# Kernel optimization log

Measured on AMD Instinct MI355X. Metric: run time of the kernel, lower is better.

Reference implementation:

```python
import jax, jax.numpy as jnp
import numpy as np

B, L, D_EMB, D_K, D_V, N_HEAD = 32, 512, 768, 512, 1024, 8
LN_EPS = 1e-6
MASK_FILL = 1e-9  # non-standard fill value from the original module


def setup_inputs() -> dict:
    key = jax.random.key(0)
    ks = jax.random.split(key, 13)
    s = 0.02
    return {
        "q": jax.random.normal(ks[0], (B, L, D_EMB), jnp.float32),
        "k": jax.random.normal(ks[1], (B, L, D_EMB), jnp.float32),
        "v": jax.random.normal(ks[2], (B, L, D_EMB), jnp.float32),
        "Wq": jax.random.normal(ks[3], (D_EMB, D_K), jnp.float32) * s,
        "Wk": jax.random.normal(ks[4], (D_EMB, D_K), jnp.float32) * s,
        "Wv": jax.random.normal(ks[5], (D_EMB, D_V), jnp.float32) * s,
        "Wconv": jax.random.normal(ks[6], (D_K, D_K), jnp.float32) * s,  # Conv1d k=1 (out_ch, in_ch)
        "bconv": jax.random.normal(ks[7], (D_K,), jnp.float32) * s,
        "Wfc": jax.random.normal(ks[8], (D_V, D_EMB), jnp.float32) * s,
        "gamma": jnp.ones((D_EMB,), jnp.float32),
        "beta": jnp.zeros((D_EMB,), jnp.float32),
        "mask1": jax.random.randint(ks[9], (B, L), 0, 2).astype(jnp.bool_),
        "mask2": jax.random.randint(ks[10], (B, L), 0, 2).astype(jnp.bool_),
    }


def reference(q, k, v, Wq, Wk, Wv, Wconv, bconv, Wfc, gamma, beta, mask1, mask2):
    Bq, Lq, _ = q.shape
    Lk = k.shape[1]
    dh_k = D_K // N_HEAD
    dh_v = D_V // N_HEAD
    residual = q

    # Q/K projections followed by the (buggy-but-faithful) Conv1d(k=1) that
    # treats the sequence axis as channels: out[b,o,l] = sum_c W[o,c]*x[b,c,l] + bias[o]
    q1 = q @ Wq                                   # (B, Lq, D_K)
    k1 = k @ Wk                                   # (B, Lk, D_K)
    q1 = jnp.einsum('oc,bcl->bol', Wconv, q1) + bconv[None, :, None]
    k1 = jnp.einsum('oc,bcl->bol', Wconv, k1) + bconv[None, :, None]
    v1 = v @ Wv                                   # (B, Lk, D_V)

    qh = q1.reshape(Bq, Lq, N_HEAD, dh_k).transpose(0, 2, 1, 3)  # (B,H,Lq,dk/H)
    kh = k1.reshape(Bq, Lk, N_HEAD, dh_k).transpose(0, 2, 1, 3)
    vh = v1.reshape(Bq, Lk, N_HEAD, dh_v).transpose(0, 2, 1, 3)

    temp = jnp.sqrt(jnp.asarray(D_K, qh.dtype))
    attn = jnp.einsum('bhqd,bhkd->bhqk', qh / temp, kh)          # (B,H,Lq,Lk)
    attn = jnp.where(mask1[:, None, :, None], MASK_FILL, attn)
    attn = jnp.where(mask2[:, None, None, :], MASK_FILL, attn)
    attn = jax.nn.softmax(attn, axis=-1)
    # dropout is identity in eval / deterministic reference

    out = jnp.einsum('bhqk,bhkd->bhqd', attn, vh)                # (B,H,Lq,dv/H)
    out = out.transpose(0, 2, 1, 3).reshape(Bq, Lq, D_V)
    out = out @ Wfc + residual                                   # (B,Lq,D_EMB)

    mu = out.mean(-1, keepdims=True)
    var = out.var(-1, keepdims=True)
    out = (out - mu) / jnp.sqrt(var + LN_EPS) * gamma + beta
    out = jnp.where(jnp.isnan(out), jnp.zeros((), out.dtype), out)
    return out, attn
```

## Files before the change

kernel.cpp:

```cpp
#include <hip/hip_runtime.h>
#include <hip/hip_fp16.h>

typedef short v8s __attribute__((ext_vector_type(8)));
typedef short v4s __attribute__((ext_vector_type(4)));
typedef float v4f __attribute__((ext_vector_type(4)));

#define BM 128
#define BN 128
#define BK 64

__device__ __forceinline__ float b2f(unsigned short u) {
    union { unsigned int i; float f; } x; x.i = ((unsigned int)u) << 16; return x.f;
}
__device__ __forceinline__ unsigned short f2b(float f) {
    union { float f; unsigned int i; } x; x.f = f;
    unsigned int r = x.i + 0x7fffu + ((x.i >> 16) & 1u);
    return (unsigned short)(r >> 16);
}

__device__ __forceinline__ void gload16(const void* g, void* l) {
    __builtin_amdgcn_global_load_lds(
        (const __attribute__((address_space(1))) void*)g,
        (__attribute__((address_space(3))) void*)l, 16, 0, 0);
}

template<int EPI>
__global__ __launch_bounds__(256)
void gemm_bt(const unsigned short* __restrict__ A, int lda, long aSB,
             const unsigned short* __restrict__ BT, int ldb, long bSB,
             void* __restrict__ C, int ldc, long cSB,
             int K,
             const float* __restrict__ bias,
             const float* __restrict__ resid, int ldr)
{
    const int z = blockIdx.z;

    __shared__ unsigned short As[BM * BK];
    __shared__ unsigned short Bs[BN * BK];

    const int tid = threadIdx.x;
    const int wave = tid >> 6, lane = tid & 63;
    const int wm = (wave >> 1) * 64, wn = (wave & 1) * 64;
    const int quad = lane >> 4, l16 = lane & 15;
    const int sx = l16 & 7;
    const int bm = blockIdx.y * BM, bn = blockIdx.x * BN;

    const unsigned short* aP[4]; const unsigned short* bP[4];
    unsigned short* lA[4]; unsigned short* lB[4];
#pragma unroll
    for (int p = 0; p < 4; p++) {
        int idx = p * 256 + tid;
        int row = idx >> 3, c = idx & 7, cc = c ^ (row & 7);
        aP[p] = A + (long)z * aSB + (long)(bm + row) * lda + cc * 8;
        bP[p] = BT + (long)z * bSB + (long)(bn + row) * ldb + cc * 8;
        lA[p] = &As[idx * 8];
        lB[p] = &Bs[idx * 8];
    }

    v4f acc[4][4] = {};

    for (int k0 = 0; k0 < K; k0 += BK) {
#pragma unroll
        for (int p = 0; p < 4; p++) {
            gload16(aP[p] + k0, lA[p]);
            gload16(bP[p] + k0, lB[p]);
        }
        __syncthreads();
#pragma unroll
        for (int ks = 0; ks < 2; ks++) {
            v8s af[4], bf[4];
#pragma unroll
            for (int i = 0; i < 4; i++) {
                const int co = ((ks * 4 + quad) ^ sx) * 8;
                af[i] = *(const v8s*)&As[(wm + i * 16 + l16) * 64 + co];
                bf[i] = *(const v8s*)&Bs[(wn + i * 16 + l16) * 64 + co];
            }
#pragma unroll
            for (int i = 0; i < 4; i++)
#pragma unroll
                for (int j = 0; j < 4; j++)
                    acc[i][j] = __builtin_amdgcn_mfma_f32_16x16x32_bf16(af[i], bf[j], acc[i][j], 0, 0, 0);
        }
        __syncthreads();
    }

    unsigned short* Cu = (unsigned short*)C + (long)z * cSB;

#pragma unroll
    for (int i = 0; i < 4; i++) {
        int rowbase = wm + i * 16 + quad * 4;
#pragma unroll
        for (int j = 0; j < 4; j++) {
            int gn = bn + wn + j * 16 + l16;
#pragma unroll
            for (int r = 0; r < 4; r++) {
                int gm = bm + rowbase + r;
                float v = acc[i][j][r];
                if (EPI == 1) {
                    int bb = gm >> 9, mm = gm & 511;
                    ((unsigned short*)C)[(long)bb * cSB + (long)gn * ldc + mm] = f2b(v);
                } else if (EPI == 2) {
                    Cu[(long)gm * ldc + gn] = f2b(v + bias[gm]);
                } else if (EPI == 4) {
                    Cu[(long)gm * ldc + gn] = f2b(v + resid[(long)gm * ldr + gn]);
                }
            }
        }
    }
}

__global__ __launch_bounds__(512, 4)
void scores_pv_k(const unsigned short* __restrict__ q1c,
                 const unsigned short* __restrict__ k1c,
                 const unsigned short* __restrict__ v1t,
                 float* __restrict__ attn,
                 unsigned short* __restrict__ out1,
                 const int* __restrict__ mask1,
                 const int* __restrict__ mask2,
                 float scale)
{
    const int id = blockIdx.x;
    const int logical = (id & 7) * 128 + (id >> 3);
    const int z = logical >> 2;
    const int bx = logical & 3;
    const int b = z >> 3, h = z & 7;

    const unsigned short* Qb = q1c + (long)b * 262144 + h * 64;
    const unsigned short* Kb = k1c + (long)b * 262144 + h * 64;
    const unsigned short* Vb = v1t + (long)b * 524288 + (long)h * 65536;

    __shared__ unsigned short KA[128 * 64];
    __shared__ unsigned short VB[128 * 128];
    __shared__ unsigned short Pl[8][640];
    __shared__ int m2s[512];

    const int tid = threadIdx.x;
    const int wave = tid >> 6, lane = tid & 63;
    const int quad = lane >> 4, l16 = lane & 15;
    const int sx = l16 & 7;
    const int bm = bx * 128;
    const int row_l = wave * 16 + l16;
    const int qrow = bm + row_l;

    m2s[tid] = mask2[b * 512 + tid];

    v8s qf0 = *(const v8s*)&Qb[(long)qrow * 512 + quad * 8];
    v8s qf1 = *(const v8s*)&Qb[(long)qrow * 512 + 32 + quad * 8];
    const int m1 = mask1[b * 512 + qrow];

    float m_l = -1e30f, sum = 0.f;

    for (int kt = 0; kt < 4; kt++) {
#pragma unroll
        for (int p = 0; p < 2; p++) {
            int idx = p * 512 + tid;
            int row = idx >> 3, c = idx & 7, cc = c ^ (row & 7);
            gload16(Kb + (long)(kt * 128 + row) * 512 + cc * 8, &KA[idx * 8]);
        }
        __syncthreads();
#pragma unroll
        for (int jl = 0; jl < 8; jl++) {
            const unsigned short* kr = &KA[(jl * 16 + l16) * 64];
            v8s kf0 = *(const v8s*)&kr[(quad ^ sx) << 3];
            v8s kf1 = *(const v8s*)&kr[((4 + quad) ^ sx) << 3];
            v4f a = (v4f){0.f, 0.f, 0.f, 0.f};
            a = __builtin_amdgcn_mfma_f32_16x16x32_bf16(kf0, qf0, a, 0, 0, 0);
            a = __builtin_amdgcn_mfma_f32_16x16x32_bf16(kf1, qf1, a, 0, 0, 0);
            int j = kt * 8 + jl;
            int4 m2v = *(const int4*)&m2s[j * 16 + quad * 4];
            float s0 = (m1 != 0 || m2v.x != 0) ? 1e-9f : a[0] * scale;
            float s1 = (m1 != 0 || m2v.y != 0) ? 1e-9f : a[1] * scale;
            float s2 = (m1 != 0 || m2v.z != 0) ? 1e-9f : a[2] * scale;
            float s3 = (m1 != 0 || m2v.w != 0) ? 1e-9f : a[3] * scale;
            float m4 = fmaxf(fmaxf(s0, s1), fmaxf(s2, s3));
            float mn = fmaxf(m_l, m4);
            sum = sum * __expf(m_l - mn)
                + (__expf(s0 - mn) + __expf(s1 - mn))
                + (__expf(s2 - mn) + __expf(s3 - mn));
            m_l = mn;
        }
        __syncthreads();
    }
    float mx = fmaxf(m_l, __shfl_xor(m_l, 16, 64));
    mx = fmaxf(mx, __shfl_xor(mx, 32, 64));
    sum *= __expf(m_l - mx);
    sum += __shfl_xor(sum, 16, 64);
    sum += __shfl_xor(sum, 32, 64);
    const float inv = 1.0f / sum;

    float* Arow = attn + (long)z * 262144 + (long)qrow * 512;
    unsigned short* Pw = &Pl[wave][l16 * 40];
    v4f acc2[8];
#pragma unroll
    for (int t = 0; t < 8; t++) acc2[t] = (v4f){0.f, 0.f, 0.f, 0.f};

    for (int kt = 0; kt < 4; kt++) {
#pragma unroll
        for (int p = 0; p < 2; p++) {
            int idx = p * 512 + tid;
            int row = idx >> 3, c = idx & 7, cc = c ^ (row & 7);
            gload16(Kb + (long)(kt * 128 + row) * 512 + cc * 8, &KA[idx * 8]);
        }
#pragma unroll
        for (int p = 0; p < 4; p++) {
            int idx = p * 512 + tid;
            int dv = idx >> 4, c = idx & 15, cc = c ^ (dv & 7);
            gload16(Vb + (long)dv * 512 + kt * 128 + cc * 8, &VB[idx * 8]);
        }
        __syncthreads();

#pragma unroll
        for (int g = 0; g < 4; g++) {
            float p8[8];
#pragma unroll
            for (int t2 = 0; t2 < 2; t2++) {
                int jl = g * 2 + t2;
                const unsigned short* kr = &KA[(jl * 16 + l16) * 64];
                v8s kf0 = *(const v8s*)&kr[(quad ^ sx) << 3];
                v8s kf1 = *(const v8s*)&kr[((4 + quad) ^ sx) << 3];
                v4f a = (v4f){0.f, 0.f, 0.f, 0.f};
                a = __builtin_amdgcn_mfma_f32_16x16x32_bf16(kf0, qf0, a, 0, 0, 0);
                a = __builtin_amdgcn_mfma_f32_16x16x32_bf16(kf1, qf1, a, 0, 0, 0);
                int j = kt * 8 + jl;
                int4 m2v = *(const int4*)&m2s[j * 16 + quad * 4];
                float s0 = (m1 != 0 || m2v.x != 0) ? 1e-9f : a[0] * scale;
                float s1 = (m1 != 0 || m2v.y != 0) ? 1e-9f : a[1] * scale;
                float s2 = (m1 != 0 || m2v.z != 0) ? 1e-9f : a[2] * scale;
                float s3 = (m1 != 0 || m2v.w != 0) ? 1e-9f : a[3] * scale;
                p8[t2 * 4 + 0] = __expf(s0 - mx) * inv;
                p8[t2 * 4 + 1] = __expf(s1 - mx) * inv;
                p8[t2 * 4 + 2] = __expf(s2 - mx) * inv;
                p8[t2 * 4 + 3] = __expf(s3 - mx) * inv;
            }
            int j0 = kt * 8 + g * 2;
            float4 w0; w0.x = p8[0]; w0.y = p8[1]; w0.z = p8[2]; w0.w = p8[3];
            float4 w1; w1.x = p8[4]; w1.y = p8[5]; w1.z = p8[6]; w1.w = p8[7];
            *(float4*)&Arow[j0 * 16 + quad * 4] = w0;
            *(float4*)&Arow[(j0 + 1) * 16 + quad * 4] = w1;
            uint2 pr0, pr1;
            pr0.x = (unsigned int)f2b(p8[0]) | ((unsigned int)f2b(p8[1]) << 16);
            pr0.y = (unsigned int)f2b(p8[2]) | ((unsigned int)f2b(p8[3]) << 16);
            pr1.x = (unsigned int)f2b(p8[4]) | ((unsigned int)f2b(p8[5]) << 16);
            pr1.y = (unsigned int)f2b(p8[6]) | ((unsigned int)f2b(p8[7]) << 16);
            *(uint2*)&Pw[quad * 4] = pr0;
            *(uint2*)&Pw[16 + quad * 4] = pr1;
            v8s pf = *(const v8s*)&Pw[quad * 8];
#pragma unroll
            for (int t = 0; t < 8; t++) {
                v8s vf = *(const v8s*)&VB[(t * 16 + l16) * 128 + (((g * 4 + quad) ^ sx) << 3)];
                acc2[t] = __builtin_amdgcn_mfma_f32_16x16x32_bf16(vf, pf, acc2[t], 0, 0, 0);
            }
        }
        __syncthreads();
    }

    unsigned short* Orow = out1 + (long)b * 524288 + (long)qrow * 1024 + h * 128;
#pragma unroll
    for (int t = 0; t < 8; t++) {
        v4s o;
        o[0] = (short)f2b(acc2[t][0]); o[1] = (short)f2b(acc2[t][1]);
        o[2] = (short)f2b(acc2[t][2]); o[3] = (short)f2b(acc2[t][3]);
        *(v4s*)&Orow[t * 16 + quad * 4] = o;
    }
}

__global__ __launch_bounds__(256)
void prep_k(const float* __restrict__ Wq, const float* __restrict__ Wk,
            const float* __restrict__ Wv, const float* __restrict__ Wfc,
            const float* __restrict__ Wconv,
            const float* __restrict__ qf, const float* __restrict__ kf,
            const float* __restrict__ vf,
            unsigned short* __restrict__ WqT, unsigned short* __restrict__ WkT,
            unsigned short* __restrict__ WvT, unsigned short* __restrict__ WfcT,
            unsigned short* __restrict__ Wconv_b,
            unsigned short* __restrict__ qb, unsigned short* __restrict__ kb,
            unsigned short* __restrict__ vb)
{
    __shared__ float t[32][33];
    int blk = blockIdx.x, tid = threadIdx.x;
    if (blk < 2304) {
        const float* src; unsigned short* dst; int K, N, local;
        if (blk < 384)       { src = Wq;  dst = WqT;  K = 768;  N = 512;  local = blk; }
        else if (blk < 768)  { src = Wk;  dst = WkT;  K = 768;  N = 512;  local = blk - 384; }
        else if (blk < 1536) { src = Wv;  dst = WvT;  K = 768;  N = 1024; local = blk - 768; }
        else                 { src = Wfc; dst = WfcT; K = 1024; N = 768;  local = blk - 1536; }
        int nb32 = N >> 5;
        int kb32 = (local / nb32) * 32, nb = (local % nb32) * 32;
        int tx = tid & 31, ty = tid >> 5;
#pragma unroll
        for (int i = 0; i < 32; i += 8)
            t[ty + i][tx] = src[(long)(kb32 + ty + i) * N + nb + tx];
        __syncthreads();
#pragma unroll
        for (int i = 0; i < 32; i += 8)
            dst[(long)(nb + ty + i) * K + kb32 + tx] = f2b(t[tx][ty + i]);
    } else if (blk < 3328) {
        int i = (blk - 2304) * 256 + tid;
        Wconv_b[i] = f2b(Wconv[i]);
    } else {
        long t0 = (long)(blk - 3328) * 4096 + (long)tid * 16;
        const float* src; unsigned short* dst; long i = t0;
        if (t0 < 12582912L)       { src = qf; dst = qb; }
        else if (t0 < 25165824L)  { src = kf; dst = kb; i = t0 - 12582912L; }
        else                      { src = vf; dst = vb; i = t0 - 25165824L; }
        float4 a = *(const float4*)&src[i];
        float4 b4 = *(const float4*)&src[i + 4];
        float4 c4 = *(const float4*)&src[i + 8];
        float4 d4 = *(const float4*)&src[i + 12];
        v8s r0, r1;
        r0[0] = (short)f2b(a.x);  r0[1] = (short)f2b(a.y);
        r0[2] = (short)f2b(a.z);  r0[3] = (short)f2b(a.w);
        r0[4] = (short)f2b(b4.x); r0[5] = (short)f2b(b4.y);
        r0[6] = (short)f2b(b4.z); r0[7] = (short)f2b(b4.w);
        r1[0] = (short)f2b(c4.x); r1[1] = (short)f2b(c4.y);
        r1[2] = (short)f2b(c4.z); r1[3] = (short)f2b(c4.w);
        r1[4] = (short)f2b(d4.x); r1[5] = (short)f2b(d4.y);
        r1[6] = (short)f2b(d4.z); r1[7] = (short)f2b(d4.w);
        *(v8s*)&dst[i] = r0;
        *(v8s*)&dst[i + 8] = r1;
    }
}

__global__ __launch_bounds__(256)
void ln_k(const unsigned short* __restrict__ x,
          const float* __restrict__ gamma,
          const float* __restrict__ beta,
          float* __restrict__ out)
{
    long row = (long)blockIdx.x * 4 + (threadIdx.x >> 6);
    int lane = threadIdx.x & 63;
    const unsigned short* p = x + row * 768;
    v8s a = *(const v8s*)&p[lane * 8];
    v4s b4 = *(const v4s*)&p[512 + lane * 4];
    float v[12];
    float s = 0.f, s2 = 0.f;
#pragma unroll
    for (int j = 0; j < 8; j++) { v[j] = b2f((unsigned short)a[j]); s += v[j]; s2 += v[j] * v[j]; }
#pragma unroll
    for (int j = 0; j < 4; j++) { v[8 + j] = b2f((unsigned short)b4[j]); s += v[8 + j]; s2 += v[8 + j] * v[8 + j]; }
#pragma unroll
    for (int o = 32; o > 0; o >>= 1) { s += __shfl_xor(s, o, 64); s2 += __shfl_xor(s2, o, 64); }
    float mean = s * (1.0f / 768.0f);
    float var = s2 * (1.0f / 768.0f) - mean * mean;
    if (!(var >= 0.f)) var = 0.f;
    float rstd = rsqrtf(var + 1e-6f);
    float o12[12];
#pragma unroll
    for (int j = 0; j < 8; j++) {
        int c = lane * 8 + j;
        float o = (v[j] - mean) * rstd * gamma[c] + beta[c];
        union { float f; unsigned int i; } uu; uu.f = o;
        if ((uu.i & 0x7FFFFFFFu) > 0x7F800000u) uu.f = 0.f;
        o12[j] = uu.f;
    }
#pragma unroll
    for (int j = 0; j < 4; j++) {
        int c = 512 + lane * 4 + j;
        float o = (v[8 + j] - mean) * rstd * gamma[c] + beta[c];
        union { float f; unsigned int i; } uu; uu.f = o;
        if ((uu.i & 0x7FFFFFFFu) > 0x7F800000u) uu.f = 0.f;
        o12[8 + j] = uu.f;
    }
    float4 f0; f0.x = o12[0]; f0.y = o12[1]; f0.z = o12[2]; f0.w = o12[3];
    float4 f1; f1.x = o12[4]; f1.y = o12[5]; f1.z = o12[6]; f1.w = o12[7];
    float4 f2; f2.x = o12[8]; f2.y = o12[9]; f2.z = o12[10]; f2.w = o12[11];
    *(float4*)&out[row * 768 + lane * 8] = f0;
    *(float4*)&out[row * 768 + lane * 8 + 4] = f1;
    *(float4*)&out[row * 768 + 512 + lane * 4] = f2;
}

extern "C" void kernel_launch(void* const* d_in, const int* in_sizes, int n_in,
                              void* d_out, int out_size, void* d_ws, size_t ws_size,
                              hipStream_t stream)
{
    const float* q     = (const float*)d_in[0];
    const float* k     = (const float*)d_in[1];
    const float* v     = (const float*)d_in[2];
    const float* Wq    = (const float*)d_in[3];
    const float* Wk    = (const float*)d_in[4];
    const float* Wv    = (const float*)d_in[5];
    const float* Wconv = (const float*)d_in[6];
    const float* bconv = (const float*)d_in[7];
    const float* Wfc   = (const float*)d_in[8];
    const float* gamma = (const float*)d_in[9];
    const float* beta  = (const float*)d_in[10];
    const int* mask1   = (const int*)d_in[11];
    const int* mask2   = (const int*)d_in[12];

    float* out  = (float*)d_out;
    float* attn = out + 12582912;

    unsigned short* ws = (unsigned short*)d_ws;
    unsigned short* WqT     = ws;
    unsigned short* WkT     = ws + 393216;
    unsigned short* WvT     = ws + 786432;
    unsigned short* WfcT    = ws + 1572864;
    unsigned short* Wconv_b = ws + 2359296;
    unsigned short* q1c     = ws + 2621440;
    unsigned short* k1c     = ws + 11010048;
    unsigned short* v1t     = ws + 19398656;
    unsigned short* out2    = ws + 19398656;

    unsigned short* aScr = (unsigned short*)attn;
    unsigned short* q1t = aScr;
    unsigned short* k1t = aScr + 8388608;
    unsigned short* qb  = aScr + 16777216;
    unsigned short* kb  = aScr + 29360128;
    unsigned short* vb  = aScr + 41943040;
    unsigned short* out1 = (unsigned short*)out;

    prep_k<<<12544, 256, 0, stream>>>(Wq, Wk, Wv, Wfc, Wconv, q, k, v,
                                      WqT, WkT, WvT, WfcT, Wconv_b, qb, kb, vb);

    const float scale = 0.04419417382415922f;

    gemm_bt<1><<<dim3(4, 128, 1), 256, 0, stream>>>(
        qb, 768, 0, WqT, 768, 0, q1t, 512, 262144, 768, nullptr, nullptr, 0);
    gemm_bt<1><<<dim3(4, 128, 1), 256, 0, stream>>>(
        kb, 768, 0, WkT, 768, 0, k1t, 512, 262144, 768, nullptr, nullptr, 0);
    gemm_bt<1><<<dim3(8, 128, 1), 256, 0, stream>>>(
        vb, 768, 0, WvT, 768, 0, v1t, 512, 524288, 768, nullptr, nullptr, 0);

    gemm_bt<2><<<dim3(4, 4, 32), 256, 0, stream>>>(
        Wconv_b, 512, 0, q1t, 512, 262144, q1c, 512, 262144, 512, bconv, nullptr, 0);
    gemm_bt<2><<<dim3(4, 4, 32), 256, 0, stream>>>(
        Wconv_b, 512, 0, k1t, 512, 262144, k1c, 512, 262144, 512, bconv, nullptr, 0);

    scores_pv_k<<<1024, 512, 0, stream>>>(
        q1c, k1c, v1t, attn, out1, mask1, mask2, scale);

    gemm_bt<4><<<dim3(6, 128, 1), 256, 0, stream>>>(
        out1, 1024, 0, WfcT, 1024, 0, out2, 768, 0, 1024, nullptr, q, 768);

    ln_k<<<4096, 256, 0, stream>>>(out2, gamma, beta, out);
}
```

Before: 708.8 us.

## Double-buffer GEMM LDS, stage transposed epilogue through LDS, merge projection launches

Refactors the bf16 MFMA GEMM into a device body that double-buffers the A/B tiles in LDS, so the next K-tile's global loads overlap the current tile's MFMAs and one barrier per iteration is removed. The transposed-output epilogue (EPI 1) now stages results in padded shared memory and writes coalesced 16-byte rows instead of scattered 2-byte stores. The three Q/K/V projections are merged into one launch, with idle blocks returning early for the narrower Q/K outputs, and the two conv GEMMs are merged into one launch. This cuts launch count and improves memory efficiency, at the cost of doubling LDS to 64KB per block, which may lower occupancy.

New measurement: 721.3 us. Within noise of the previous version (+1.8%).

```diff
diff --git a/kernel.cpp b/kernel.cpp
--- a/kernel.cpp
+++ b/kernel.cpp
@@ -1,5 +1,4 @@
 #include <hip/hip_runtime.h>
-#include <hip/hip_fp16.h>
 
 typedef short v8s __attribute__((ext_vector_type(8)));
 typedef short v4s __attribute__((ext_vector_type(4)));
@@ -22,6 +21,123 @@
     __builtin_amdgcn_global_load_lds(
         (const __attribute__((address_space(1))) void*)g,
         (__attribute__((address_space(3))) void*)l, 16, 0, 0);
+}
+
+template<int EPI>
+__device__ __forceinline__ void gemm_body(
+    const unsigned short* __restrict__ A, int lda, long aOff,
+    const unsigned short* __restrict__ BT, int ldb, long bOff,
+    void* __restrict__ C, int ldc, long cOff, long cSBt,
+    int K, const float* __restrict__ bias,
+    const float* __restrict__ resid, int ldr,
+    int bm, int bn)
+{
+    __shared__ unsigned short SM[32768];
+
+    const int tid = threadIdx.x;
+    const int wave = tid >> 6, lane = tid & 63;
+    const int wm = (wave >> 1) * 64, wn = (wave & 1) * 64;
+    const int quad = lane >> 4, l16 = lane & 15;
+    const int sx = l16 & 7;
+
+    const unsigned short* aP[4]; const unsigned short* bP[4];
+    int ldsOff[4];
+#pragma unroll
+    for (int p = 0; p < 4; p++) {
+        int idx = p * 256 + tid;
+        int row = idx >> 3, c = idx & 7, cc = c ^ (row & 7);
+        aP[p] = A + aOff + (long)(bm + row) * lda + cc * 8;
+        bP[p] = BT + bOff + (long)(bn + row) * ldb + cc * 8;
+        ldsOff[p] = idx * 8;
+    }
+
+    auto stage = [&](int t, int b) {
+        const int k0 = t * BK;
+        unsigned short* base = &SM[b * 16384];
+#pragma unroll
+        for (int p = 0; p < 4; p++) {
+            gload16(aP[p] + k0, base + ldsOff[p]);
+            gload16(bP[p] + k0, base + 8192 + ldsOff[p]);
+        }
+    };
+
+    v4f acc[4][4] = {};
+    const int nt = K >> 6;
+
+    stage(0, 0);
+    __syncthreads();
+
+    int buf = 0;
+    for (int t = 0; t < nt; t++) {
+        if (t + 1 < nt) stage(t + 1, buf ^ 1);
+        const unsigned short* As = &SM[buf * 16384];
+        const unsigned short* Bs = As + 8192;
+#pragma unroll
+        for (int ks = 0; ks < 2; ks++) {
+            v8s af[4], bf[4];
+#pragma unroll
+            for (int i = 0; i < 4; i++) {
+                const int co = ((ks * 4 + quad) ^ sx) * 8;
+                af[i] = *(const v8s*)&As[(wm + i * 16 + l16) * 64 + co];
+                bf[i] = *(const v8s*)&Bs[(wn + i * 16 + l16) * 64 + co];
+            }
+#pragma unroll
+            for (int i = 0; i < 4; i++)
+#pragma unroll
+                for (int j = 0; j < 4; j++)
+                    acc[i][j] = __builtin_amdgcn_mfma_f32_16x16x32_bf16(af[i], bf[j], acc[i][j], 0, 0, 0);
+        }
+        __syncthreads();
+        buf ^= 1;
+    }
+
+    if (EPI == 1) {
+        unsigned short* T = SM;
+#pragma unroll
+        for (int i = 0; i < 4; i++) {
+            int mb = wm + i * 16 + quad * 4;
+#pragma unroll
+            for (int j = 0; j < 4; j++) {
+                int n = wn + j * 16 + l16;
+                unsigned int lo = (unsigned int)f2b(acc[i][j][0]) | ((unsigned int)f2b(acc[i][j][1]) << 16);
+                unsigned int hi = (unsigned int)f2b(acc[i][j][2]) | ((unsigned int)f2b(acc[i][j][3]) << 16);
+                *(unsigned int*)&T[n * 136 + mb] = lo;
+                *(unsigned int*)&T[n * 136 + mb + 2] = hi;
+            }
+        }
+        __syncthreads();
+        const int bb = bm >> 9, mm0 = bm & 511;
+        unsigned short* Cu = (unsigned short*)C + cOff + (long)bb * cSBt + mm0;
+#pragma unroll
+        for (int cch = 0; cch < 2; cch++) {
+            int idx = cch * 256 + tid;
+            int row = idx >> 2, part = idx & 3;
+            const uint4* s = (const uint4*)&T[row * 136 + part * 32];
+            uint4 v0 = s[0], v1 = s[1], v2 = s[2], v3 = s[3];
+            uint4* d = (uint4*)&Cu[(long)(bn + row) * ldc + part * 32];
+            d[0] = v0; d[1] = v1; d[2] = v2; d[3] = v3;
+        }
+    } else {
+        unsigned short* Cu = (unsigned short*)C + cOff;
+#pragma unroll
+        for (int i = 0; i < 4; i++) {
+            int rowbase = wm + i * 16 + quad * 4;
+#pragma unroll
+            for (int j = 0; j < 4; j++) {
+                int gn = bn + wn + j * 16 + l16;
+#pragma unroll
+                for (int r = 0; r < 4; r++) {
+                    int gm = bm + rowbase + r;
+                    float v = acc[i][j][r];
+                    if (EPI == 2) {
+                        Cu[(long)gm * ldc + gn] = f2b(v + bias[gm]);
+                    } else if (EPI == 4) {
+                        Cu[(long)gm * ldc + gn] = f2b(v + resid[(long)gm * ldr + gn]);
+                    }
+                }
+            }
+        }
+    }
 }
 
 template<int EPI>
@@ -29,84 +145,52 @@
 void gemm_bt(const unsigned short* __restrict__ A, int lda, long aSB,
              const unsigned short* __restrict__ BT, int ldb, long bSB,
              void* __restrict__ C, int ldc, long cSB,
-             int K,
-             const float* __restrict__ bias,
+             int K, const float* __restrict__ bias,
              const float* __restrict__ resid, int ldr)
 {
     const int z = blockIdx.z;
-
-    __shared__ unsigned short As[BM * BK];
-    __shared__ unsigned short Bs[BN * BK];
-
-    const int tid = threadIdx.x;
-    const int wave = tid >> 6, lane = tid & 63;
-    const int wm = (wave >> 1) * 64, wn = (wave & 1) * 64;
-    const int quad = lane >> 4, l16 = lane & 15;
-    const int sx = l16 & 7;
+    gemm_body<EPI>(A, lda, (long)z * aSB, BT, ldb, (long)z * bSB,
+                   C, ldc, (long)z * cSB, cSB, K, bias, resid, ldr,
+                   blockIdx.y * BM, blockIdx.x * BN);
+}
+
+__global__ __launch_bounds__(256)
+void proj3_k(const unsigned short* __restrict__ qb, const unsigned short* __restrict__ kb,
+             const unsigned short* __restrict__ vb,
+             const unsigned short* __restrict__ WqT, const unsigned short* __restrict__ WkT,
+             const unsigned short* __restrict__ WvT,
+             unsigned short* __restrict__ q1t, unsigned short* __restrict__ k1t,
+             unsigned short* __restrict__ v1t)
+{
+    const int cfg = blockIdx.z;
     const int bm = blockIdx.y * BM, bn = blockIdx.x * BN;
-
-    const unsigned short* aP[4]; const unsigned short* bP[4];
-    unsigned short* lA[4]; unsigned short* lB[4];
-#pragma unroll
-    for (int p = 0; p < 4; p++) {
-        int idx = p * 256 + tid;
-        int row = idx >> 3, c = idx & 7, cc = c ^ (row & 7);
-        aP[p] = A + (long)z * aSB + (long)(bm + row) * lda + cc * 8;
-        bP[p] = BT + (long)z * bSB + (long)(bn + row) * ldb + cc * 8;
-        lA[p] = &As[idx * 8];
-        lB[p] = &Bs[idx * 8];
-    }
-
-    v4f acc[4][4] = {};
-
-    for (int k0 = 0; k0 < K; k0 += BK) {
-#pragma unroll
-        for (int p = 0; p < 4; p++) {
-            gload16(aP[p] + k0, lA[p]);
-            gload16(bP[p] + k0, lB[p]);
-        }
-        __syncthreads();
-#pragma unroll
-        for (int ks = 0; ks < 2; ks++) {
-            v8s af[4], bf[4];
-#pragma unroll
-            for (int i = 0; i < 4; i++) {
-                const int co = ((ks * 4 + quad) ^ sx) * 8;
-                af[i] = *(const v8s*)&As[(wm + i * 16 + l16) * 64 + co];
-                bf[i] = *(const v8s*)&Bs[(wn + i * 16 + l16) * 64 + co];
-            }
-#pragma unroll
-            for (int i = 0; i < 4; i++)
-#pragma unroll
-                for (int j = 0; j < 4; j++)
-                    acc[i][j] = __builtin_amdgcn_mfma_f32_16x16x32_bf16(af[i], bf[j], acc[i][j], 0, 0, 0);
-        }
-        __syncthreads();
-    }
-
-    unsigned short* Cu = (unsigned short*)C + (long)z * cSB;
-
-#pragma unroll
-    for (int i = 0; i < 4; i++) {
-        int rowbase = wm + i * 16 + quad * 4;
-#pragma unroll
-        for (int j = 0; j < 4; j++) {
-            int gn = bn + wn + j * 16 + l16;
-#pragma unroll
-            for (int r = 0; r < 4; r++) {
-                int gm = bm + rowbase + r;
-                float v = acc[i][j][r];
-                if (EPI == 1) {
-                    int bb = gm >> 9, mm = gm & 511;
-                    ((unsigned short*)C)[(long)bb * cSB + (long)gn * ldc + mm] = f2b(v);
-                } else if (EPI == 2) {
-                    Cu[(long)gm * ldc + gn] = f2b(v + bias[gm]);
-                } else if (EPI == 4) {
-                    Cu[(long)gm * ldc + gn] = f2b(v + resid[(long)gm * ldr + gn]);
-                }
-            }
-        }
-    }
+    if (cfg == 0) {
+        if (blockIdx.x >= 4) return;
+        gemm_body<1>(qb, 768, 0, WqT, 768, 0, q1t, 512, 0, 262144, 768,
+                     nullptr, nullptr, 0, bm, bn);
+    } else if (cfg == 1) {
+        if (blockIdx.x >= 4) return;
+        gemm_body<1>(kb, 768, 0, WkT, 768, 0, k1t, 512, 0, 262144, 768,
+                     nullptr, nullptr, 0, bm, bn);
+    } else {
+        gemm_body<1>(vb, 768, 0, WvT, 768, 0, v1t, 512, 0, 524288, 768,
+                     nullptr, nullptr, 0, bm, bn);
+    }
+}
+
+__global__ __launch_bounds__(256)
+void conv2_k(const unsigned short* __restrict__ Wconv_b,
+             const unsigned short* __restrict__ q1t, const unsigned short* __restrict__ k1t,
+             unsigned short* __restrict__ q1c, unsigned short* __restrict__ k1c,
+             const float* __restrict__ bconv)
+{
+    const int z = blockIdx.z;
+    const int b = z & 31, sel = z >> 5;
+    const int bm = blockIdx.y * BM, bn = blockIdx.x * BN;
+    const unsigned short* Bt = sel ? k1t : q1t;
+    unsigned short* Cc = sel ? k1c : q1c;
+    gemm_body<2>(Wconv_b, 512, 0, Bt, 512, (long)b * 262144,
+                 Cc, 512, (long)b * 262144, 0, 512, bconv, nullptr, 0, bm, bn);
 }
 
 __global__ __launch_bounds__(512, 4)
@@ -414,17 +498,11 @@
 
     const float scale = 0.04419417382415922f;
 
-    gemm_bt<1><<<dim3(4, 128, 1), 256, 0, stream>>>(
-        qb, 768, 0, WqT, 768, 0, q1t, 512, 262144, 768, nullptr, nullptr, 0);
-    gemm_bt<1><<<dim3(4, 128, 1), 256, 0, stream>>>(
-        kb, 768, 0, WkT, 768, 0, k1t, 512, 262144, 768, nullptr, nullptr, 0);
-    gemm_bt<1><<<dim3(8, 128, 1), 256, 0, stream>>>(
-        vb, 768, 0, WvT, 768, 0, v1t, 512, 524288, 768, nullptr, nullptr, 0);
-
-    gemm_bt<2><<<dim3(4, 4, 32), 256, 0, stream>>>(
-        Wconv_b, 512, 0, q1t, 512, 262144, q1c, 512, 262144, 512, bconv, nullptr, 0);
-    gemm_bt<2><<<dim3(4, 4, 32), 256, 0, stream>>>(
-        Wconv_b, 512, 0, k1t, 512, 262144, k1c, 512, 262144, 512, bconv, nullptr, 0);
+    proj3_k<<<dim3(8, 128, 3), 256, 0, stream>>>(
+        qb, kb, vb, WqT, WkT, WvT, q1t, k1t, v1t);
+
+    conv2_k<<<dim3(4, 4, 64), 256, 0, stream>>>(
+        Wconv_b, q1t, k1t, q1c, k1c, bconv);
 
     scores_pv_k<<<1024, 512, 0, stream>>>(
         q1c, k1c, v1t, attn, out1, mask1, mask2, scale);
```
